# Optimization experiments

Measured on AMD Instinct MI355X. Metric: run time of the kernel, lower is better.

Reference implementation:

```python
import jax, jax.numpy as jnp
import numpy as np

N_TETS, C, D = 1_000_000, 32, 8
N_FACES = 400_000


def setup_inputs() -> dict:
    key = jax.random.key(0)
    features = jax.random.normal(key, (N_TETS, C, D), dtype=jnp.float32)
    # disjoint face pairs: arange gives all-distinct tet indices (< N_TETS)
    faces = jnp.arange(N_FACES * 2, dtype=jnp.int64).reshape(N_FACES, 2)
    return {"features": features, "faces": faces}


def reference(features, faces):
    # Per-tet max over the local feature axis D: [n_tets, C]
    base = jnp.max(features, axis=-1)
    # For each sampled face, max over concat([tet1, tet2], dim=-1) ==
    # elementwise max of the two per-tet maxima. Gather both endpoints.
    f1 = base[faces[:, 0]]            # [n_faces, C]
    f2 = base[faces[:, 1]]            # [n_faces, C]
    shared = jnp.maximum(f1, f2)      # [n_faces, C]
    # Scatter shared features back to both tets (faces are disjoint, no races)
    out = base.at[faces[:, 0]].set(shared).at[faces[:, 1]].set(shared)
    return out
```

## Files before the change

### kernel.cpp

```cpp
#include <hip/hip_runtime.h>


__global__ void partner_init_kernel(int* __restrict__ partner, int n) {
    int stride = gridDim.x * blockDim.x;
    for (int i = blockIdx.x * blockDim.x + threadIdx.x; i < n; i += stride)
        partner[i] = -1;
}

__global__ void partner_build_kernel(const int* __restrict__ faces,
                                     int* __restrict__ partner, int n_faces) {
    int stride = gridDim.x * blockDim.x;
    for (int f = blockIdx.x * blockDim.x + threadIdx.x; f < n_faces; f += stride) {
        int a = faces[2 * f];
        int b = faces[2 * f + 1];
        partner[a] = b;
        partner[b] = a;
    }
}

__global__ void fused_pool_kernel(const float* __restrict__ feat,
                                  const int* __restrict__ partner,
                                  float* __restrict__ out, int n) {
    int stride = gridDim.x * blockDim.x;
    for (int t = blockIdx.x * blockDim.x + threadIdx.x; t < n; t += stride) {
        const float4* p = reinterpret_cast<const float4*>(feat + (size_t)t * 8);
        float4 a = p[0];
        float4 b = p[1];
        float m = fmaxf(fmaxf(fmaxf(a.x, a.y), fmaxf(a.z, a.w)),
                        fmaxf(fmaxf(b.x, b.y), fmaxf(b.z, b.w)));
        int row = t >> 5;
        int pr  = partner[row];
        if (pr >= 0) {
            int c = t & 31;
            const float4* q =
                reinterpret_cast<const float4*>(feat + ((size_t)pr * 32 + c) * 8);
            float4 x = q[0];
            float4 y = q[1];
            float m2 = fmaxf(fmaxf(fmaxf(x.x, x.y), fmaxf(x.z, x.w)),
                             fmaxf(fmaxf(y.x, y.y), fmaxf(y.z, y.w)));
            m = fmaxf(m, m2);
        }
        out[t] = m;
    }
}


__global__ void base_max_kernel(const float* __restrict__ feat,
                                float* __restrict__ out, int n) {
    int stride = gridDim.x * blockDim.x;
    for (int i = blockIdx.x * blockDim.x + threadIdx.x; i < n; i += stride) {
        const float4* p = reinterpret_cast<const float4*>(feat + (size_t)i * 8);
        float4 a = p[0];
        float4 b = p[1];
        float m = fmaxf(fmaxf(fmaxf(a.x, a.y), fmaxf(a.z, a.w)),
                        fmaxf(fmaxf(b.x, b.y), fmaxf(b.z, b.w)));
        out[i] = m;
    }
}

__global__ void face_share_kernel(const int* __restrict__ faces,
                                  float* __restrict__ out, int n_faces) {
    int total = n_faces * 8;
    int stride = gridDim.x * blockDim.x;
    for (int t = blockIdx.x * blockDim.x + threadIdx.x; t < total; t += stride) {
        int face = t >> 3;
        int c4   = (t & 7) << 2;
        size_t f1 = (size_t)faces[2 * face];
        size_t f2 = (size_t)faces[2 * face + 1];
        float* p1 = out + f1 * 32 + c4;
        float* p2 = out + f2 * 32 + c4;
        float4 v1 = *reinterpret_cast<const float4*>(p1);
        float4 v2 = *reinterpret_cast<const float4*>(p2);
        float4 s;
        s.x = fmaxf(v1.x, v2.x);
        s.y = fmaxf(v1.y, v2.y);
        s.z = fmaxf(v1.z, v2.z);
        s.w = fmaxf(v1.w, v2.w);
        *reinterpret_cast<float4*>(p1) = s;
        *reinterpret_cast<float4*>(p2) = s;
    }
}

extern "C" void kernel_launch(void* const* d_in, const int* in_sizes, int n_in,
                              void* d_out, int out_size, void* d_ws, size_t ws_size,
                              hipStream_t stream) {
    const float* feat  = (const float*)d_in[0];
    const int*   faces = (const int*)d_in[1];
    float* out = (float*)d_out;

    const int n_elems = out_size;
    const int n_rows  = out_size / 32;
    const int n_faces = in_sizes[1] / 2;

    const int block = 256;
    const size_t partner_bytes = (size_t)n_rows * sizeof(int);

    if (ws_size >= partner_bytes) {
        int* partner = (int*)d_ws;

        int grid_i = min((n_rows + block - 1) / block, 2048);
        partner_init_kernel<<<grid_i, block, 0, stream>>>(partner, n_rows);

        int grid_f = min((n_faces + block - 1) / block, 2048);
        partner_build_kernel<<<grid_f, block, 0, stream>>>(faces, partner, n_faces);

        int grid_m = min((n_elems + block - 1) / block, 4096);
        fused_pool_kernel<<<grid_m, block, 0, stream>>>(feat, partner, out, n_elems);
    } else {
        int grid_a = min((n_elems + block - 1) / block, 4096);
        base_max_kernel<<<grid_a, block, 0, stream>>>(feat, out, n_elems);

        int grid_b = min((n_faces * 8 + block - 1) / block, 4096);
        face_share_kernel<<<grid_b, block, 0, stream>>>(faces, out, n_faces);
    }
}
```

Measured before the change: 249.4 us.

## Process four channels per thread and share adjacent-row maxima via warp shuffle

Each thread now handles four consecutive channels of a row and writes one float4 output. When a tet's partner is the adjacent row (row^1), the partner maxima come from a lane 8 positions away via __shfl_xor instead of a second global read. This targets the duplicate reads of partner features, roughly halving feature traffic for the arange-style face layout. Non-adjacent partners still fall back to a global gather, and the shuffle correctness relies on the row pair sitting within the same 64-lane wavefront.

New measurement: 251.6 us. About the same (+0.9%).

```diff
diff --git a/kernel.cpp b/kernel.cpp
--- a/kernel.cpp
+++ b/kernel.cpp
@@ -18,29 +18,48 @@
     }
 }
 
+__device__ __forceinline__ float max8(float4 a, float4 b) {
+    return fmaxf(fmaxf(fmaxf(a.x, a.y), fmaxf(a.z, a.w)),
+                 fmaxf(fmaxf(b.x, b.y), fmaxf(b.z, b.w)));
+}
+
 __global__ void fused_pool_kernel(const float* __restrict__ feat,
                                   const int* __restrict__ partner,
-                                  float* __restrict__ out, int n) {
+                                  float* __restrict__ out, int n4) {
     int stride = gridDim.x * blockDim.x;
-    for (int t = blockIdx.x * blockDim.x + threadIdx.x; t < n; t += stride) {
-        const float4* p = reinterpret_cast<const float4*>(feat + (size_t)t * 8);
-        float4 a = p[0];
-        float4 b = p[1];
-        float m = fmaxf(fmaxf(fmaxf(a.x, a.y), fmaxf(a.z, a.w)),
-                        fmaxf(fmaxf(b.x, b.y), fmaxf(b.z, b.w)));
-        int row = t >> 5;
-        int pr  = partner[row];
+    for (int t = blockIdx.x * blockDim.x + threadIdx.x; t < n4; t += stride) {
+        int row = t >> 3;
+        int c4  = (t & 7) << 2;
+        const float4* p =
+            reinterpret_cast<const float4*>(feat + (size_t)row * 256 + (size_t)c4 * 8);
+        float m[4];
+#pragma unroll
+        for (int j = 0; j < 4; ++j)
+            m[j] = max8(p[2 * j], p[2 * j + 1]);
+
+        int pr = partner[row];
+
+        float pm[4];
+#pragma unroll
+        for (int j = 0; j < 4; ++j)
+            pm[j] = __shfl_xor(m[j], 8, 64);
+
         if (pr >= 0) {
-            int c = t & 31;
-            const float4* q =
-                reinterpret_cast<const float4*>(feat + ((size_t)pr * 32 + c) * 8);
-            float4 x = q[0];
-            float4 y = q[1];
-            float m2 = fmaxf(fmaxf(fmaxf(x.x, x.y), fmaxf(x.z, x.w)),
-                             fmaxf(fmaxf(y.x, y.y), fmaxf(y.z, y.w)));
-            m = fmaxf(m, m2);
+            if (pr == (row ^ 1)) {
+#pragma unroll
+                for (int j = 0; j < 4; ++j)
+                    m[j] = fmaxf(m[j], pm[j]);
+            } else {
+                const float4* q = reinterpret_cast<const float4*>(
+                    feat + (size_t)pr * 256 + (size_t)c4 * 8);
+#pragma unroll
+                for (int j = 0; j < 4; ++j)
+                    m[j] = fmaxf(m[j], max8(q[2 * j], q[2 * j + 1]));
+            }
         }
-        out[t] = m;
+
+        float4 o = make_float4(m[0], m[1], m[2], m[3]);
+        *reinterpret_cast<float4*>(out + (size_t)t * 4) = o;
     }
 }
 
@@ -50,11 +69,7 @@
     int stride = gridDim.x * blockDim.x;
     for (int i = blockIdx.x * blockDim.x + threadIdx.x; i < n; i += stride) {
         const float4* p = reinterpret_cast<const float4*>(feat + (size_t)i * 8);
-        float4 a = p[0];
-        float4 b = p[1];
-        float m = fmaxf(fmaxf(fmaxf(a.x, a.y), fmaxf(a.z, a.w)),
-                        fmaxf(fmaxf(b.x, b.y), fmaxf(b.z, b.w)));
-        out[i] = m;
+        out[i] = max8(p[0], p[1]);
     }
 }
 
@@ -104,8 +119,9 @@
         int grid_f = min((n_faces + block - 1) / block, 2048);
         partner_build_kernel<<<grid_f, block, 0, stream>>>(faces, partner, n_faces);
 
-        int grid_m = min((n_elems + block - 1) / block, 4096);
-        fused_pool_kernel<<<grid_m, block, 0, stream>>>(feat, partner, out, n_elems);
+        int n4 = n_elems / 4;
+        int grid_m = min((n4 + block - 1) / block, 4096);
+        fused_pool_kernel<<<grid_m, block, 0, stream>>>(feat, partner, out, n4);
     } else {
         int grid_a = min((n_elems + block - 1) / block, 4096);
         base_max_kernel<<<grid_a, block, 0, stream>>>(feat, out, n_elems);
```
